# Performance work log

Hardware: AMD Instinct MI355X
Metric: run time of the kernel (lower is better)

Reference implementation:

```python
import jax, jax.numpy as jnp
import numpy as np

VOXEL_LENGTH = 1.2


def grid_sample_3d_border(vol, grid):
    """torch.nn.functional.grid_sample (5D, bilinear, align_corners=False,
    padding_mode='border') with grid flattened to (B, N, 3) in (x, y, z) order.
    vol: (B, C, D, H, W). Returns (B, C, N)."""

    def sample_one(v, g):
        C, D, H, W = v.shape
        x, y, z = g[:, 0], g[:, 1], g[:, 2]
        # align_corners=False unnormalization
        ix = ((x + 1.0) * W - 1.0) * 0.5
        iy = ((y + 1.0) * H - 1.0) * 0.5
        iz = ((z + 1.0) * D - 1.0) * 0.5
        ix0f, iy0f, iz0f = jnp.floor(ix), jnp.floor(iy), jnp.floor(iz)
        wx, wy, wz = ix - ix0f, iy - iy0f, iz - iz0f
        # border padding: clamp indices, keep unclamped weights
        x0 = jnp.clip(ix0f, 0, W - 1).astype(jnp.int32)
        x1 = jnp.clip(ix0f + 1, 0, W - 1).astype(jnp.int32)
        y0 = jnp.clip(iy0f, 0, H - 1).astype(jnp.int32)
        y1 = jnp.clip(iy0f + 1, 0, H - 1).astype(jnp.int32)
        z0 = jnp.clip(iz0f, 0, D - 1).astype(jnp.int32)
        z1 = jnp.clip(iz0f + 1, 0, D - 1).astype(jnp.int32)
        vflat = v.reshape(C, D * H * W)

        def gather(zi, yi, xi):  # -> (C, N)
            return vflat[:, (zi * H + yi) * W + xi]

        out = (
            gather(z0, y0, x0) * ((1 - wz) * (1 - wy) * (1 - wx))
            + gather(z0, y0, x1) * ((1 - wz) * (1 - wy) * wx)
            + gather(z0, y1, x0) * ((1 - wz) * wy * (1 - wx))
            + gather(z0, y1, x1) * ((1 - wz) * wy * wx)
            + gather(z1, y0, x0) * (wz * (1 - wy) * (1 - wx))
            + gather(z1, y0, x1) * (wz * (1 - wy) * wx)
            + gather(z1, y1, x0) * (wz * wy * (1 - wx))
            + gather(z1, y1, x1) * (wz * wy * wx)
        )
        return out

    return jax.vmap(sample_one)(vol, grid)


def setup_inputs() -> dict:
    key = jax.random.key(0)
    ks = jax.random.split(key, 16)
    B, IMG, STEPS = 2, 64, 24
    N = IMG * IMG * STEPS
    C_IN, HID, RES = 32, 256, 32
    # points in world space, inside the voxel cube [-0.6, 0.6]
    points = jax.random.uniform(ks[0], (B, N, 3), jnp.float32) * 1.2 - 0.6
    feature_volume = jax.random.normal(ks[1], (B, C_IN, RES, RES, RES), jnp.float32)

    def lin(k, fan_in, fan_out, scale):
        kw, kb = jax.random.split(k)
        W = jax.random.uniform(kw, (fan_out, fan_in), jnp.float32, -scale, scale)
        b = jax.random.uniform(kb, (fan_out,), jnp.float32, -scale, scale)
        return W, b

    freq = 12.0
    W0, b0 = lin(ks[2], C_IN, HID, 1.0 / C_IN)  # first_layer_film_sine_init
    W1, b1 = lin(ks[3], HID, HID, float(np.sqrt(6.0 / HID) / freq))
    W2, b2 = lin(ks[4], HID, HID, float(np.sqrt(6.0 / HID) / freq))
    W3, b3 = lin(ks[5], HID, HID, float(np.sqrt(6.0 / HID) / freq))
    Wf, bf = lin(ks[6], HID, 4, float(np.sqrt(6.0 / HID) / freq))
    return {
        "points": points, "feature_volume": feature_volume,
        "W0": W0, "b0": b0, "W1": W1, "b1": b1, "W2": W2, "b2": b2,
        "W3": W3, "b3": b3, "Wf": Wf, "bf": bf,
        "img_size": 64, "num_steps": 24,
    }


def reference(points, feature_volume, W0, b0, W1, b1, W2, b2, W3, b3, Wf, bf,
              img_size, num_steps):
    grid = points / (VOXEL_LENGTH / 2.0)  # (B, N, 3) in [-1, 1]
    feats = grid_sample_3d_border(feature_volume, grid)  # (B, C, N)
    x = feats.transpose(0, 2, 1)  # (B, N, C)
    for W, b in ((W0, b0), (W1, b1), (W2, b2), (W3, b3)):
        x = jnp.sin(jnp.einsum('bnc,hc->bnh', x, W) + b)
    rgb_sigma = jnp.einsum('bnh,oh->bno', x, Wf) + bf  # (B, N, 4)
    rgb = jax.nn.sigmoid(rgb_sigma[..., :3])
    sigma = rgb_sigma[..., 3:4]
    return jnp.concatenate([rgb, sigma], axis=-1)
```

## Files before the change

kernel.cpp:

```cpp
#include <hip/hip_runtime.h>
#include <math.h>

#define THREADS 256

typedef __attribute__((ext_vector_type(8))) short bf16x8;
typedef __attribute__((ext_vector_type(4))) float f32x4;

#define NCHUNK 26
#define STREAM_BYTES (NCHUNK * 16384)

__device__ __host__ __forceinline__ int sigma_k(int k) {
    return (k & 0xE1) | ((k & 0x04) << 2) | ((k & 0x18) >> 1) | (k & 0x02);
}

__device__ __forceinline__ ushort f2bf(float f) {
    union { float f; unsigned u; } v; v.f = f;
    unsigned r = v.u + 0x7FFFu + ((v.u >> 16) & 1u);
    return (ushort)(r >> 16);
}

__device__ __forceinline__ float fast_sigmoid(float x) {
    return 1.0f / (1.0f + __expf(-x));
}

__device__ __forceinline__ unsigned cvt_pk_bf16(float lo, float hi) {
    unsigned d;
    asm("v_cvt_pk_bf16_f32 %0, %1, %2" : "=v"(d) : "v"(lo), "v"(hi));
    return d;
}

__global__ void build_frags(const float* __restrict__ W0,
                            const float* __restrict__ W1,
                            const float* __restrict__ W2,
                            const float* __restrict__ W3,
                            const float* __restrict__ Wf,
                            ushort* __restrict__ stream) {
    const int gid = blockIdx.x * 256 + threadIdx.x;
    const int f = gid >> 6;
    if (f >= 416) return;
    const int lane = gid & 63;
    const int p16 = lane & 15, g = lane >> 4;
    ushort* dst = stream + (size_t)f * 512 + lane * 8;

    if (f < 16) {
        const float* row = W0 + (size_t)(f * 16 + p16) * 32;
#pragma unroll
        for (int i = 0; i < 8; ++i) dst[i] = f2bf(row[8 * g + i]);
    } else if (f < 400) {
        const int t = f - 16;
        const int h = t >> 7;
        const int r = t & 127;
        const int sub = r >> 4;
        const int idx = r & 15;
        const int q = sub & 1;
        const int kq = sub >> 1;
        const int ksl = idx >> 3;
        const int ntl = idx & 7;
        const int nt = q * 8 + ntl;
        const int ks = kq * 2 + ksl;
        const float* W = (h == 0) ? W1 : (h == 1) ? W2 : W3;
        const float* row = W + (size_t)(nt * 16 + p16) * 256;
#pragma unroll
        for (int i = 0; i < 8; ++i) dst[i] = f2bf(row[sigma_k(32 * ks + 8 * g + i)]);
    } else if (f < 408) {
        const int ks = f - 400;
        if (p16 < 4) {
            const float* row = Wf + (size_t)p16 * 256;
#pragma unroll
            for (int i = 0; i < 8; ++i) dst[i] = f2bf(row[sigma_k(32 * ks + 8 * g + i)]);
        } else {
#pragma unroll
            for (int i = 0; i < 8; ++i) dst[i] = 0;
        }
    } else {
#pragma unroll
        for (int i = 0; i < 8; ++i) dst[i] = 0;
    }
}

__global__ void vol_chlast(const float* __restrict__ vol, float* __restrict__ dst, int nvox) {
    int v = blockIdx.x * 256 + threadIdx.x;
    if (v >= nvox) return;
    const int b = v >> 15, idx = v & 32767;
    const float* s = vol + (size_t)b * 32 * 32768 + idx;
    float* d = dst + (size_t)v * 32;
#pragma unroll
    for (int c = 0; c < 32; ++c) d[c] = s[(size_t)c * 32768];
}

#define MF(a, b, c) __builtin_amdgcn_mfma_f32_16x16x32_bf16((a), (b), (c), 0, 0, 0)

__global__ __launch_bounds__(THREADS, 2)
void siren_pl(const float* __restrict__ points,
              const float* __restrict__ vol,
              const float* __restrict__ b0, const float* __restrict__ b1,
              const float* __restrict__ b2, const float* __restrict__ b3,
              const float* __restrict__ bfin,
              const ushort* __restrict__ Wstream,
              const float* __restrict__ volcl, int use_cl,
              float* __restrict__ out, long long total, int N) {
    __shared__ ushort ring[2][8192];

    const int tid = (int)threadIdx.x;
    const int w = tid >> 6;
    const int lane = tid & 63;
    const int p16 = lane & 15;
    const int g = lane >> 4;

    const long long base = (long long)blockIdx.x * 128;

    auto stage = [&](int c) {
        if (c >= NCHUNK) return;
        const ushort* src = Wstream + (size_t)c * 8192;
        ushort* dstbase = &ring[c & 1][0];
#pragma unroll
        for (int q = 0; q < 4; ++q) {
            const int off = (q * 4 + w) * 512;
            __builtin_amdgcn_global_load_lds(
                (const __attribute__((address_space(1))) unsigned int*)(src + off + lane * 8),
                (__attribute__((address_space(3))) unsigned int*)(dstbase + off),
                16, 0, 0);
        }
    };
    stage(0);
    stage(1);

    bf16x8 af0[2];
    {
#pragma unroll
        for (int ptt = 0; ptt < 2; ++ptt) {
            const long long gidx = base + w * 32 + ptt * 16 + p16;
            const long long gp = gidx < total ? gidx : total - 1;
            const int bi = (int)(gp / N);
            const float* pp = points + gp * 3;
            const float sc = 1.0f / 0.6f;
            const float ix = (pp[0] * sc + 1.0f) * 16.0f - 0.5f;
            const float iy = (pp[1] * sc + 1.0f) * 16.0f - 0.5f;
            const float iz = (pp[2] * sc + 1.0f) * 16.0f - 0.5f;
            const float fx = floorf(ix), fy = floorf(iy), fz = floorf(iz);
            const float wx = ix - fx, wy = iy - fy, wz = iz - fz;
            const int x0 = (int)fminf(fmaxf(fx, 0.0f), 31.0f);
            const int x1 = (int)fminf(fmaxf(fx + 1.0f, 0.0f), 31.0f);
            const int y0 = (int)fminf(fmaxf(fy, 0.0f), 31.0f);
            const int y1 = (int)fminf(fmaxf(fy + 1.0f, 0.0f), 31.0f);
            const int z0 = (int)fminf(fmaxf(fz, 0.0f), 31.0f);
            const int z1 = (int)fminf(fmaxf(fz + 1.0f, 0.0f), 31.0f);
            const int i000 = (z0 * 32 + y0) * 32 + x0, i001 = (z0 * 32 + y0) * 32 + x1;
            const int i010 = (z0 * 32 + y1) * 32 + x0, i011 = (z0 * 32 + y1) * 32 + x1;
            const int i100 = (z1 * 32 + y0) * 32 + x0, i101 = (z1 * 32 + y0) * 32 + x1;
            const int i110 = (z1 * 32 + y1) * 32 + x0, i111 = (z1 * 32 + y1) * 32 + x1;
            const float omx = 1.0f - wx, omy = 1.0f - wy, omz = 1.0f - wz;
            const float w000 = omz * omy * omx, w001 = omz * omy * wx;
            const float w010 = omz * wy * omx,  w011 = omz * wy * wx;
            const float w100 = wz * omy * omx,  w101 = wz * omy * wx;
            const float w110 = wz * wy * omx,   w111 = wz * wy * wx;

            f32x4 a[2];
            if (use_cl) {
                const float* vb = volcl + (size_t)bi * 32768 * 32 + g * 8;
#pragma unroll
                for (int h = 0; h < 2; ++h) {
                    const float* vh = vb + h * 4;
                    a[h]  = w000 * *(const f32x4*)(vh + (size_t)i000 * 32);
                    a[h] += w001 * *(const f32x4*)(vh + (size_t)i001 * 32);
                    a[h] += w010 * *(const f32x4*)(vh + (size_t)i010 * 32);
                    a[h] += w011 * *(const f32x4*)(vh + (size_t)i011 * 32);
                    a[h] += w100 * *(const f32x4*)(vh + (size_t)i100 * 32);
                    a[h] += w101 * *(const f32x4*)(vh + (size_t)i101 * 32);
                    a[h] += w110 * *(const f32x4*)(vh + (size_t)i110 * 32);
                    a[h] += w111 * *(const f32x4*)(vh + (size_t)i111 * 32);
                }
            } else {
                const float* vb = vol + ((size_t)bi * 32 + (size_t)g * 8) * 32768;
#pragma unroll
                for (int c = 0; c < 8; ++c) {
                    const float* vc = vb + (size_t)c * 32768;
                    a[c >> 2][c & 3] =
                        vc[i000] * w000 + vc[i001] * w001 + vc[i010] * w010 + vc[i011] * w011 +
                        vc[i100] * w100 + vc[i101] * w101 + vc[i110] * w110 + vc[i111] * w111;
                }
            }
            union { bf16x8 v; unsigned u[4]; } pk;
            pk.u[0] = cvt_pk_bf16(a[0][0], a[0][1]);
            pk.u[1] = cvt_pk_bf16(a[0][2], a[0][3]);
            pk.u[2] = cvt_pk_bf16(a[1][0], a[1][1]);
            pk.u[3] = cvt_pk_bf16(a[1][2], a[1][3]);
            af0[ptt] = pk.v;
        }
    }

    f32x4 accA[2][8];
    f32x4 accB[2][8];
    bf16x8 bfr[2][8];

    auto frag_at = [&](int slot, int idx) -> bf16x8 {
        return *(const bf16x8*)&ring[slot][idx * 512 + lane * 8];
    };
    auto init_half = [&](f32x4 (&A)[2][8], const float* __restrict__ b, int ntbase) {
#pragma unroll
        for (int m = 0; m < 8; ++m) {
            const f32x4 bv = *(const f32x4*)&b[(ntbase + m) * 16 + 4 * g];
            A[0][m] = bv; A[1][m] = bv;
        }
    };
    auto pack_half = [&](f32x4 (&A)[2][8], int ksbase) {
#pragma unroll
        for (int ptt = 0; ptt < 2; ++ptt)
#pragma unroll
            for (int ks2 = 0; ks2 < 4; ++ks2) {
                union { bf16x8 v; unsigned u[4]; } pk;
#pragma unroll
                for (int j = 0; j < 4; ++j) {
                    const int m = 2 * ks2 + (j >> 1);
                    const int r = 2 * (j & 1);
                    pk.u[j] = cvt_pk_bf16(__sinf(A[ptt][m][r]), __sinf(A[ptt][m][r + 1]));
                }
                bfr[ptt][ksbase + ks2] = pk.v;
            }
    };
    auto chunk_mfma = [&](int slot, int kq, f32x4 (&A)[2][8]) {
        __builtin_amdgcn_s_setprio(1);
#pragma unroll
        for (int ksl = 0; ksl < 2; ++ksl) {
            const bf16x8 bA = bfr[0][kq * 2 + ksl];
            const bf16x8 bB = bfr[1][kq * 2 + ksl];
#pragma unroll
            for (int ntl = 0; ntl < 8; ++ntl) {
                const bf16x8 wfr = frag_at(slot, ksl * 8 + ntl);
                A[0][ntl] = MF(wfr, bA, A[0][ntl]);
                A[1][ntl] = MF(wfr, bB, A[1][ntl]);
            }
        }
        __builtin_amdgcn_s_setprio(0);
    };

    init_half(accA, b0, 0);
    init_half(accB, b0, 8);
    __syncthreads();

    __builtin_amdgcn_s_setprio(1);
#pragma unroll
    for (int ntl = 0; ntl < 8; ++ntl) {
        const bf16x8 wl = frag_at(0, ntl);
        const bf16x8 wh = frag_at(0, 8 + ntl);
        accA[0][ntl] = MF(wl, af0[0], accA[0][ntl]);
        accA[1][ntl] = MF(wl, af0[1], accA[1][ntl]);
        accB[0][ntl] = MF(wh, af0[0], accB[0][ntl]);
        accB[1][ntl] = MF(wh, af0[1], accB[1][ntl]);
    }
    __builtin_amdgcn_s_setprio(0);
    __syncthreads(); stage(2);

#define LAYER(cbase, bnext_lo, bnext_hi)                               \
    do {                                                               \
        pack_half(accA, 0); init_half(accA, bnext_lo, 0);              \
        chunk_mfma((cbase) & 1, 0, accA);                              \
        __syncthreads(); stage((cbase) + 2);                           \
        pack_half(accB, 4); init_half(accB, bnext_hi, 8);              \
        chunk_mfma((cbase + 1) & 1, 0, accB);                          \
        __syncthreads(); stage((cbase) + 3);                           \
        chunk_mfma((cbase + 2) & 1, 1, accA);                          \
        __syncthreads(); stage((cbase) + 4);                           \
        chunk_mfma((cbase + 3) & 1, 1, accB);                          \
        __syncthreads(); stage((cbase) + 5);                           \
        chunk_mfma((cbase + 4) & 1, 2, accA);                          \
        __syncthreads(); stage((cbase) + 6);                           \
        chunk_mfma((cbase + 5) & 1, 2, accB);                          \
        __syncthreads(); stage((cbase) + 7);                           \
        chunk_mfma((cbase + 6) & 1, 3, accA);                          \
        __syncthreads(); stage((cbase) + 8);                           \
        chunk_mfma((cbase + 7) & 1, 3, accB);                          \
        __syncthreads(); stage((cbase) + 9);                           \
    } while (0)

    LAYER(1, b1, b1);
    LAYER(9, b2, b2);
    LAYER(17, b3, b3);

    pack_half(accA, 0);
    pack_half(accB, 4);
    {
        f32x4 fo[2] = {{0, 0, 0, 0}, {0, 0, 0, 0}};
#pragma unroll
        for (int ks = 0; ks < 8; ++ks) {
            const bf16x8 wfr = frag_at(25 & 1, ks);
            fo[0] = MF(wfr, bfr[0][ks], fo[0]);
            fo[1] = MF(wfr, bfr[1][ks], fo[1]);
        }
        if (g == 0) {
#pragma unroll
            for (int ptt = 0; ptt < 2; ++ptt) {
                const long long oi = base + w * 32 + ptt * 16 + p16;
                if (oi < total) {
                    float4 o;
                    o.x = fast_sigmoid(fo[ptt][0] + bfin[0]);
                    o.y = fast_sigmoid(fo[ptt][1] + bfin[1]);
                    o.z = fast_sigmoid(fo[ptt][2] + bfin[2]);
                    o.w = fo[ptt][3] + bfin[3];
                    *(float4*)(out + oi * 4) = o;
                }
            }
        }
    }
}

extern "C" void kernel_launch(void* const* d_in, const int* in_sizes, int n_in,
                              void* d_out, int out_size, void* d_ws, size_t ws_size,
                              hipStream_t stream) {
    const float* points = (const float*)d_in[0];
    const float* vol    = (const float*)d_in[1];
    const float* W0 = (const float*)d_in[2];
    const float* b0 = (const float*)d_in[3];
    const float* W1 = (const float*)d_in[4];
    const float* b1 = (const float*)d_in[5];
    const float* W2 = (const float*)d_in[6];
    const float* b2 = (const float*)d_in[7];
    const float* W3 = (const float*)d_in[8];
    const float* b3 = (const float*)d_in[9];
    const float* Wf = (const float*)d_in[10];
    const float* bf = (const float*)d_in[11];

    const int B = in_sizes[1] / (32 * 32 * 32 * 32);
    const int N = in_sizes[0] / (3 * B);
    const long long total = (long long)B * N;
    const int tiles = (int)((total + 127) / 128);

    ushort* Wstream = (ushort*)d_ws;
    build_frags<<<104, 256, 0, stream>>>(W0, W1, W2, W3, Wf, Wstream);

    const int use_cl = (ws_size >= (size_t)STREAM_BYTES + (size_t)B * 32768 * 32 * 4) ? 1 : 0;
    float* volcl = (float*)((char*)d_ws + STREAM_BYTES);
    if (use_cl) {
        const int nvox = B * 32768;
        vol_chlast<<<(nvox + 255) / 256, 256, 0, stream>>>(vol, volcl, nvox);
    }

    siren_pl<<<tiles, THREADS, 0, stream>>>(
        points, vol, b0, b1, b2, b3, bf, Wstream, volcl, use_cl,
        (float*)d_out, total, N);
}
```

Measured before the change: 107.1 us.

## Use native v_sin with prescaled weights and reorder layer halves for overlap

Weights and biases are prescaled by 1/(2π) at fragment-build time so the hidden activations can go through the raw v_sin_f32 instruction, skipping the range reduction done by __sinf. The weight stream is reordered so each layer first finishes all K chunks for the low half of the outputs, then for the high half. This lets the sine packing of one half overlap with MFMAs of the other and shortens the dependency at layer boundaries. It adds a small bias-scaling kernel and workspace region. It also relies on the hardware sine being accurate enough in the revolutions domain for the pre-activation magnitudes seen here.

```diff
diff --git a/kernel.cpp b/kernel.cpp
--- a/kernel.cpp
+++ b/kernel.cpp
@@ -6,8 +6,11 @@
 typedef __attribute__((ext_vector_type(8))) short bf16x8;
 typedef __attribute__((ext_vector_type(4))) float f32x4;
 
+#define INV2PI 0.15915494309189535f
+
 #define NCHUNK 26
 #define STREAM_BYTES (NCHUNK * 16384)
+#define SBIAS_BYTES 4096
 
 __device__ __host__ __forceinline__ int sigma_k(int k) {
     return (k & 0xE1) | ((k & 0x04) << 2) | ((k & 0x18) >> 1) | (k & 0x02);
@@ -27,6 +30,12 @@
     unsigned d;
     asm("v_cvt_pk_bf16_f32 %0, %1, %2" : "=v"(d) : "v"(lo), "v"(hi));
     return d;
+}
+
+__device__ __forceinline__ float hw_sin(float x) {
+    float r;
+    asm("v_sin_f32 %0, %1" : "=v"(r) : "v"(x));
+    return r;
 }
 
 __global__ void build_frags(const float* __restrict__ W0,
@@ -45,15 +54,15 @@
     if (f < 16) {
         const float* row = W0 + (size_t)(f * 16 + p16) * 32;
 #pragma unroll
-        for (int i = 0; i < 8; ++i) dst[i] = f2bf(row[8 * g + i]);
+        for (int i = 0; i < 8; ++i) dst[i] = f2bf(row[8 * g + i] * INV2PI);
     } else if (f < 400) {
         const int t = f - 16;
         const int h = t >> 7;
         const int r = t & 127;
         const int sub = r >> 4;
         const int idx = r & 15;
-        const int q = sub & 1;
-        const int kq = sub >> 1;
+        const int q = sub >> 2;
+        const int kq = sub & 3;
         const int ksl = idx >> 3;
         const int ntl = idx & 7;
         const int nt = q * 8 + ntl;
@@ -61,7 +70,7 @@
         const float* W = (h == 0) ? W1 : (h == 1) ? W2 : W3;
         const float* row = W + (size_t)(nt * 16 + p16) * 256;
 #pragma unroll
-        for (int i = 0; i < 8; ++i) dst[i] = f2bf(row[sigma_k(32 * ks + 8 * g + i)]);
+        for (int i = 0; i < 8; ++i) dst[i] = f2bf(row[sigma_k(32 * ks + 8 * g + i)] * INV2PI);
     } else if (f < 408) {
         const int ks = f - 400;
         if (p16 < 4) {
@@ -76,6 +85,15 @@
 #pragma unroll
         for (int i = 0; i < 8; ++i) dst[i] = 0;
     }
+}
+
+__global__ void scale_biases(const float* __restrict__ b0, const float* __restrict__ b1,
+                             const float* __restrict__ b2, const float* __restrict__ b3,
+                             float* __restrict__ sb) {
+    const int i = blockIdx.x * 256 + threadIdx.x;
+    const int l = i >> 8, j = i & 255;
+    const float* b = (l == 0) ? b0 : (l == 1) ? b1 : (l == 2) ? b2 : b3;
+    sb[i] = b[j] * INV2PI;
 }
 
 __global__ void vol_chlast(const float* __restrict__ vol, float* __restrict__ dst, int nvox) {
@@ -93,10 +111,9 @@
 __global__ __launch_bounds__(THREADS, 2)
 void siren_pl(const float* __restrict__ points,
               const float* __restrict__ vol,
-              const float* __restrict__ b0, const float* __restrict__ b1,
-              const float* __restrict__ b2, const float* __restrict__ b3,
               const float* __restrict__ bfin,
               const ushort* __restrict__ Wstream,
+              const float* __restrict__ sb,
               const float* __restrict__ volcl, int use_cl,
               float* __restrict__ out, long long total, int N) {
     __shared__ ushort ring[2][8192];
@@ -213,7 +230,7 @@
                 for (int j = 0; j < 4; ++j) {
                     const int m = 2 * ks2 + (j >> 1);
                     const int r = 2 * (j & 1);
-                    pk.u[j] = cvt_pk_bf16(__sinf(A[ptt][m][r]), __sinf(A[ptt][m][r + 1]));
+                    pk.u[j] = cvt_pk_bf16(hw_sin(A[ptt][m][r]), hw_sin(A[ptt][m][r + 1]));
                 }
                 bfr[ptt][ksbase + ks2] = pk.v;
             }
@@ -234,8 +251,12 @@
         __builtin_amdgcn_s_setprio(0);
     };
 
-    init_half(accA, b0, 0);
-    init_half(accB, b0, 8);
+    const float* sb1 = sb;
+    const float* sb2 = sb + 256;
+    const float* sb3 = sb + 512;
+
+    init_half(accA, sb, 0);
+    init_half(accB, sb, 8);
     __syncthreads();
 
     __builtin_amdgcn_s_setprio(1);
@@ -251,38 +272,47 @@
     __builtin_amdgcn_s_setprio(0);
     __syncthreads(); stage(2);
 
-#define LAYER(cbase, bnext_lo, bnext_hi)                               \
-    do {                                                               \
-        pack_half(accA, 0); init_half(accA, bnext_lo, 0);              \
-        chunk_mfma((cbase) & 1, 0, accA);                              \
-        __syncthreads(); stage((cbase) + 2);                           \
-        pack_half(accB, 4); init_half(accB, bnext_hi, 8);              \
-        chunk_mfma((cbase + 1) & 1, 0, accB);                          \
-        __syncthreads(); stage((cbase) + 3);                           \
-        chunk_mfma((cbase + 2) & 1, 1, accA);                          \
-        __syncthreads(); stage((cbase) + 4);                           \
-        chunk_mfma((cbase + 3) & 1, 1, accB);                          \
-        __syncthreads(); stage((cbase) + 5);                           \
-        chunk_mfma((cbase + 4) & 1, 2, accA);                          \
-        __syncthreads(); stage((cbase) + 6);                           \
-        chunk_mfma((cbase + 5) & 1, 2, accB);                          \
-        __syncthreads(); stage((cbase) + 7);                           \
-        chunk_mfma((cbase + 6) & 1, 3, accA);                          \
-        __syncthreads(); stage((cbase) + 8);                           \
-        chunk_mfma((cbase + 7) & 1, 3, accB);                          \
-        __syncthreads(); stage((cbase) + 9);                           \
-    } while (0)
-
-    LAYER(1, b1, b1);
-    LAYER(9, b2, b2);
-    LAYER(17, b3, b3);
-
     pack_half(accA, 0);
-    pack_half(accB, 4);
+    init_half(accA, sb + 256, 0);
+
+    auto layer = [&](int ib, const float* sbL, const float* sbN) {
+        pack_half(accB, 4);
+        init_half(accB, sbL, 8);
+        chunk_mfma(ib & 1, 0, accA);
+        __syncthreads(); stage(ib + 2);
+        chunk_mfma((ib + 1) & 1, 1, accA);
+        __syncthreads(); stage(ib + 3);
+        chunk_mfma((ib + 2) & 1, 2, accA);
+        __syncthreads(); stage(ib + 4);
+        chunk_mfma((ib + 3) & 1, 3, accA);
+        __syncthreads(); stage(ib + 5);
+        pack_half(accA, 0);
+        if (sbN) init_half(accA, sbN, 0);
+        chunk_mfma((ib + 4) & 1, 0, accB);
+        __syncthreads(); stage(ib + 6);
+        chunk_mfma((ib + 5) & 1, 1, accB);
+        __syncthreads(); stage(ib + 7);
+        chunk_mfma((ib + 6) & 1, 2, accB);
+        __syncthreads(); stage(ib + 8);
+        chunk_mfma((ib + 7) & 1, 3, accB);
+        __syncthreads(); stage(ib + 9);
+    };
+
+    layer(1,  sb + 256, sb + 512);
+    layer(9,  sb + 512, sb + 768);
+    layer(17, sb + 768, nullptr);
+
     {
         f32x4 fo[2] = {{0, 0, 0, 0}, {0, 0, 0, 0}};
 #pragma unroll
-        for (int ks = 0; ks < 8; ++ks) {
+        for (int ks = 0; ks < 4; ++ks) {
+            const bf16x8 wfr = frag_at(25 & 1, ks);
+            fo[0] = MF(wfr, bfr[0][ks], fo[0]);
+            fo[1] = MF(wfr, bfr[1][ks], fo[1]);
+        }
+        pack_half(accB, 4);
+#pragma unroll
+        for (int ks = 4; ks < 8; ++ks) {
             const bf16x8 wfr = frag_at(25 & 1, ks);
             fo[0] = MF(wfr, bfr[0][ks], fo[0]);
             fo[1] = MF(wfr, bfr[1][ks], fo[1]);
@@ -326,16 +356,19 @@
     const int tiles = (int)((total + 127) / 128);
 
     ushort* Wstream = (ushort*)d_ws;
+    float* sb = (float*)((char*)d_ws + STREAM_BYTES);
     build_frags<<<104, 256, 0, stream>>>(W0, W1, W2, W3, Wf, Wstream);
-
-    const int use_cl = (ws_size >= (size_t)STREAM_BYTES + (size_t)B * 32768 * 32 * 4) ? 1 : 0;
-    float* volcl = (float*)((char*)d_ws + STREAM_BYTES);
+    scale_biases<<<4, 256, 0, stream>>>(b0, b1, b2, b3, sb);
+
+    const size_t fixed = (size_t)STREAM_BYTES + SBIAS_BYTES;
+    const int use_cl = (ws_size >= fixed + (size_t)B * 32768 * 32 * 4) ? 1 : 0;
+    float* volcl = (float*)((char*)d_ws + fixed);
     if (use_cl) {
         const int nvox = B * 32768;
         vol_chlast<<<(nvox + 255) / 256, 256, 0, stream>>>(vol, volcl, nvox);
     }
 
     siren_pl<<<tiles, THREADS, 0, stream>>>(
-        points, vol, b0, b1, b2, b3, bf, Wstream, volcl, use_cl,
+        points, vol, bf, Wstream, sb, volcl, use_cl,
         (float*)d_out, total, N);
 }
```

New measurement: 106.8 us. About the same (-0.3%).
